# Kernel tuning notes

Measured on AMD Instinct MI355X. Metric: run time of the kernel, lower is better.

## Reference

```python
import jax, jax.numpy as jnp
import numpy as np

B, C, D, H, W = 8, 512, 512, 128, 128


def setup_inputs() -> dict:
    key = jax.random.key(0)
    ks = jax.random.split(key, 6)
    s = 0.02  # small init scale for stable softmax
    return {
        "x": jax.random.normal(ks[0], (B, C, H, W), dtype=jnp.float32),
        "context": jax.random.normal(ks[1], (B, D), dtype=jnp.float32),
        "Wq": jax.random.normal(ks[2], (C, D), dtype=jnp.float32) * s,
        "bq": jnp.ones((C,), dtype=jnp.float32),
        "Wk": jax.random.normal(ks[3], (C, C), dtype=jnp.float32) * s,
        "bk": jnp.zeros((C,), dtype=jnp.float32),
        "Wv": jax.random.normal(ks[4], (C, C), dtype=jnp.float32) * s,
        "bv": jnp.zeros((C,), dtype=jnp.float32),
    }


def reference(x, context, Wq, bq, Wk, bk, Wv, bv):
    # x: (B,C,H,W), context: (B,D)
    scale = x.shape[1] ** (-0.5)
    # q_proj: Linear(D -> C), single query per batch element
    q = context @ Wq.T + bq                      # (B, C)
    # 1x1 convs are channel-mixing GEMMs over the spatial grid
    k = jnp.einsum('bchw,oc->bohw', x, Wk) + bk[None, :, None, None]  # (B,C,H,W)
    v = jnp.einsum('bchw,oc->bohw', x, Wv) + bv[None, :, None, None]  # (B,C,H,W)
    # attention logits over the HW positions (query length == 1)
    logits = jnp.einsum('bc,bchw->bhw', q, k) * scale                 # (B,H,W)
    Bn, Hn, Wn = logits.shape
    attn = jax.nn.softmax(logits.reshape(Bn, Hn * Wn), axis=-1).reshape(Bn, Hn, Wn)
    # attention-pooled value -> channel gate
    gate = jnp.einsum('bhw,bchw->bc', attn, v)                        # (B,C)
    return x * gate[:, :, None, None]
```

## Files before the change

kernel.cpp:

```cpp
#include <hip/hip_runtime.h>
#include <math.h>

#define BB   8
#define CC   512
#define DD   512
#define HW   16384
#define HW4  4096


__global__ __launch_bounds__(256) void k_qproj(const float* __restrict__ ctx,
                                               const float* __restrict__ Wq,
                                               const float* __restrict__ bq,
                                               float* __restrict__ q) {
    int t = blockIdx.x * 256 + threadIdx.x;
    int b = t >> 9, c = t & (CC - 1);
    const float4* cr = (const float4*)(ctx + (size_t)b * DD);
    const float4* wr = (const float4*)(Wq + (size_t)c * DD);
    float acc = 0.f;
    #pragma unroll 8
    for (int d = 0; d < DD / 4; ++d) {
        float4 a = cr[d], w = wr[d];
        acc += a.x * w.x + a.y * w.y + a.z * w.z + a.w * w.w;
    }
    q[t] = acc + bq[c];
}

__global__ __launch_bounds__(256) void k_qk(const float* __restrict__ q,
                                            const float* __restrict__ Wk,
                                            float* __restrict__ qk) {
    __shared__ float qs[CC];
    int b = blockIdx.x >> 1;
    int c = (blockIdx.x & 1) * 256 + threadIdx.x;
    for (int i = threadIdx.x; i < CC; i += 256) qs[i] = q[b * CC + i];
    __syncthreads();
    float acc = 0.f;
    #pragma unroll 8
    for (int o = 0; o < CC; ++o) acc += qs[o] * Wk[(size_t)o * CC + c];
    qk[b * CC + c] = acc;
}

__global__ __launch_bounds__(256) void k_logits(const float* __restrict__ x,
                                                const float* __restrict__ qk,
                                                float* __restrict__ logits) {
    __shared__ float qs[CC];
    __shared__ float4 part[3][64];
    int b       = blockIdx.x >> 6;
    int hwchunk = blockIdx.x & 63;
    int wave = threadIdx.x >> 6, lane = threadIdx.x & 63;
    int hw4 = hwchunk * 64 + lane;
    for (int i = threadIdx.x; i < CC; i += 256) qs[i] = qk[b * CC + i];
    __syncthreads();
    const float4* x4 = (const float4*)x;
    size_t base = (size_t)b * CC * HW4 + (size_t)(wave * 128) * HW4 + hw4;
    float ax = 0.f, ay = 0.f, az = 0.f, aw = 0.f;
    #pragma unroll 8
    for (int c = 0; c < 128; ++c) {
        float4 v = x4[base + (size_t)c * HW4];
        float w = qs[wave * 128 + c];
        ax += w * v.x; ay += w * v.y; az += w * v.z; aw += w * v.w;
    }
    if (wave > 0) {
        float4 p = { ax, ay, az, aw };
        part[wave - 1][lane] = p;
    }
    __syncthreads();
    if (wave == 0) {
        #pragma unroll
        for (int w2 = 0; w2 < 3; ++w2) {
            float4 p = part[w2][lane];
            ax += p.x; ay += p.y; az += p.z; aw += p.w;
        }
        const float scale = 0.04419417382415922f;
        float4 o = { ax * scale, ay * scale, az * scale, aw * scale };
        ((float4*)logits)[(size_t)b * HW4 + hw4] = o;
    }
}

__global__ __launch_bounds__(1024) void k_softmax(float* __restrict__ buf) {
    int b = blockIdx.x, tid = threadIdx.x;
    float4* p4 = (float4*)(buf + (size_t)b * HW);
    float4 v[4];
    float m = -1e30f;
    #pragma unroll
    for (int i = 0; i < 4; ++i) {
        v[i] = p4[tid + i * 1024];
        m = fmaxf(m, fmaxf(fmaxf(v[i].x, v[i].y), fmaxf(v[i].z, v[i].w)));
    }
    __shared__ float redm[16], reds[16];
    for (int off = 32; off; off >>= 1) m = fmaxf(m, __shfl_down(m, off));
    if ((tid & 63) == 0) redm[tid >> 6] = m;
    __syncthreads();
    if (tid < 64) {
        float mm = (tid < 16) ? redm[tid] : -1e30f;
        for (int off = 8; off; off >>= 1) mm = fmaxf(mm, __shfl_down(mm, off));
        if (tid == 0) redm[0] = mm;
    }
    __syncthreads();
    m = redm[0];
    float s = 0.f;
    #pragma unroll
    for (int i = 0; i < 4; ++i) {
        v[i].x = expf(v[i].x - m); v[i].y = expf(v[i].y - m);
        v[i].z = expf(v[i].z - m); v[i].w = expf(v[i].w - m);
        s += v[i].x + v[i].y + v[i].z + v[i].w;
    }
    for (int off = 32; off; off >>= 1) s += __shfl_down(s, off);
    if ((tid & 63) == 0) reds[tid >> 6] = s;
    __syncthreads();
    if (tid < 64) {
        float ss = (tid < 16) ? reds[tid] : 0.f;
        for (int off = 8; off; off >>= 1) ss += __shfl_down(ss, off);
        if (tid == 0) reds[0] = ss;
    }
    __syncthreads();
    float inv = 1.f / reds[0];
    #pragma unroll
    for (int i = 0; i < 4; ++i) {
        float4 o = { v[i].x * inv, v[i].y * inv, v[i].z * inv, v[i].w * inv };
        p4[tid + i * 1024] = o;
    }
}

__global__ __launch_bounds__(256) void k_pool(const float* __restrict__ x,
                                              const float* __restrict__ attn,
                                              float* __restrict__ pooled) {
    int bc = blockIdx.x;
    int b  = bc >> 9;
    int tid = threadIdx.x;
    const float4* xr = (const float4*)x    + (size_t)bc * HW4;
    const float4* ar = (const float4*)attn + (size_t)b  * HW4;
    float acc = 0.f;
    #pragma unroll 8
    for (int i = tid; i < HW4; i += 256) {
        float4 xv = xr[i], av = ar[i];
        acc += xv.x * av.x + xv.y * av.y + xv.z * av.z + xv.w * av.w;
    }
    for (int off = 32; off; off >>= 1) acc += __shfl_down(acc, off);
    __shared__ float red[4];
    if ((tid & 63) == 0) red[tid >> 6] = acc;
    __syncthreads();
    if (tid == 0) pooled[bc] = red[0] + red[1] + red[2] + red[3];
}

__global__ __launch_bounds__(256) void k_gate(const float* __restrict__ pooled,
                                              const float* __restrict__ Wv,
                                              const float* __restrict__ bv,
                                              float* __restrict__ gate) {
    int t = blockIdx.x * 256 + threadIdx.x;
    int b = t >> 9, o = t & (CC - 1);
    const float4* pr = (const float4*)(pooled + (size_t)b * CC);
    const float4* wr = (const float4*)(Wv + (size_t)o * CC);
    float acc = 0.f;
    #pragma unroll 8
    for (int i = 0; i < CC / 4; ++i) {
        float4 p = pr[i], w = wr[i];
        acc += p.x * w.x + p.y * w.y + p.z * w.z + p.w * w.w;
    }
    gate[t] = acc + bv[o];
}

__global__ __launch_bounds__(256) void k_out(const float* __restrict__ x,
                                             const float* __restrict__ gate,
                                             float* __restrict__ out) {
    int bc = blockIdx.x;
    float g = gate[bc];
    const float4* xr = (const float4*)x   + (size_t)bc * HW4;
    float4*       orow = (float4*)out     + (size_t)bc * HW4;
    #pragma unroll 8
    for (int i = threadIdx.x; i < HW4; i += 256) {
        float4 v = xr[i];
        float4 o = { v.x * g, v.y * g, v.z * g, v.w * g };
        orow[i] = o;
    }
}

extern "C" void kernel_launch(void* const* d_in, const int* in_sizes, int n_in,
                              void* d_out, int out_size, void* d_ws, size_t ws_size,
                              hipStream_t stream) {
    const float* x   = (const float*)d_in[0];
    const float* ctx = (const float*)d_in[1];
    const float* Wq  = (const float*)d_in[2];
    const float* bq  = (const float*)d_in[3];
    const float* Wk  = (const float*)d_in[4];
    const float* Wv  = (const float*)d_in[6];
    const float* bv  = (const float*)d_in[7];
    float* out = (float*)d_out;

    float* ws     = (float*)d_ws;
    float* q      = ws;
    float* qk     = ws + 4096;
    float* pooled = ws + 8192;
    float* gate   = ws + 12288;
    float* logits = ws + 16384;

    k_qproj  <<<  16, 256, 0, stream>>>(ctx, Wq, bq, q);
    k_qk     <<<  16, 256, 0, stream>>>(q, Wk, qk);
    k_logits <<< 512, 256, 0, stream>>>(x, qk, logits);
    k_softmax<<<  BB,1024, 0, stream>>>(logits);
    k_pool   <<<4096, 256, 0, stream>>>(x, logits, pooled);
    k_gate   <<<  16, 256, 0, stream>>>(pooled, Wv, bv, gate);
    k_out    <<<4096, 256, 0, stream>>>(x, gate, out);
}
```

Before: 616.6 us.

## Fuse logits, softmax and pooling with per-chunk online-softmax partials

Replaces the logits, softmax and pooling kernels with one kernel. Each block computes its chunk of logits, a local max and exp-sum, and then re-reads its x tile (likely still in cache) to produce per-channel partial pooled sums. A small combine kernel rescales the chunk partials flash-attention style. This removes the separate full pass over x in k_pool and the logits round trip, at the cost of per-channel wave shuffle reductions and a 64-way partial buffer.

After: 643.2 us. 1.04x slower.

```diff
diff --git a/kernel.cpp b/kernel.cpp
--- a/kernel.cpp
+++ b/kernel.cpp
@@ -6,6 +6,7 @@
 #define DD   512
 #define HW   16384
 #define HW4  4096
+#define NCHUNK 64
 
 
 __global__ __launch_bounds__(256) void k_qproj(const float* __restrict__ ctx,
@@ -39,15 +40,18 @@
     qk[b * CC + c] = acc;
 }
 
-__global__ __launch_bounds__(256) void k_logits(const float* __restrict__ x,
-                                                const float* __restrict__ qk,
-                                                float* __restrict__ logits) {
-    __shared__ float qs[CC];
-    __shared__ float4 part[3][64];
-    int b       = blockIdx.x >> 6;
-    int hwchunk = blockIdx.x & 63;
+__global__ __launch_bounds__(256) void k_fused(const float* __restrict__ x,
+                                               const float* __restrict__ qk,
+                                               float* __restrict__ part,
+                                               float* __restrict__ stats) {
+    __shared__ float  qs[CC];
+    __shared__ float4 comb[3][64];
+    __shared__ float4 p4s[64];
+    __shared__ float  partLDS[CC];
+    int b     = blockIdx.x >> 6;
+    int chunk = blockIdx.x & 63;
     int wave = threadIdx.x >> 6, lane = threadIdx.x & 63;
-    int hw4 = hwchunk * 64 + lane;
+    int hw4 = chunk * 64 + lane;
     for (int i = threadIdx.x; i < CC; i += 256) qs[i] = qk[b * CC + i];
     __syncthreads();
     const float4* x4 = (const float4*)x;
@@ -61,85 +65,69 @@
     }
     if (wave > 0) {
         float4 p = { ax, ay, az, aw };
-        part[wave - 1][lane] = p;
+        comb[wave - 1][lane] = p;
     }
     __syncthreads();
     if (wave == 0) {
         #pragma unroll
         for (int w2 = 0; w2 < 3; ++w2) {
-            float4 p = part[w2][lane];
+            float4 p = comb[w2][lane];
             ax += p.x; ay += p.y; az += p.z; aw += p.w;
         }
         const float scale = 0.04419417382415922f;
-        float4 o = { ax * scale, ay * scale, az * scale, aw * scale };
-        ((float4*)logits)[(size_t)b * HW4 + hw4] = o;
+        ax *= scale; ay *= scale; az *= scale; aw *= scale;
+        float m = fmaxf(fmaxf(ax, ay), fmaxf(az, aw));
+        #pragma unroll
+        for (int off = 32; off; off >>= 1) m = fmaxf(m, __shfl_xor(m, off));
+        float4 p;
+        p.x = expf(ax - m); p.y = expf(ay - m);
+        p.z = expf(az - m); p.w = expf(aw - m);
+        float s = p.x + p.y + p.z + p.w;
+        #pragma unroll
+        for (int off = 32; off; off >>= 1) s += __shfl_xor(s, off);
+        p4s[lane] = p;
+        if (lane == 0) { stats[blockIdx.x * 2] = m; stats[blockIdx.x * 2 + 1] = s; }
     }
+    __syncthreads();
+    float4 pv = p4s[lane];
+    #pragma unroll 4
+    for (int c = 127; c >= 0; --c) {
+        float4 v = x4[base + (size_t)c * HW4];
+        float r = pv.x * v.x + pv.y * v.y + pv.z * v.z + pv.w * v.w;
+        #pragma unroll
+        for (int off = 32; off; off >>= 1) r += __shfl_down(r, off);
+        if (lane == 0) partLDS[wave * 128 + c] = r;
+    }
+    __syncthreads();
+    float4* pr = (float4*)(part + (size_t)blockIdx.x * CC);
+    for (int i = threadIdx.x; i < CC / 4; i += 256) pr[i] = ((float4*)partLDS)[i];
 }
 
-__global__ __launch_bounds__(1024) void k_softmax(float* __restrict__ buf) {
+__global__ __launch_bounds__(256) void k_combine(const float* __restrict__ part,
+                                                 const float* __restrict__ stats,
+                                                 float* __restrict__ pooled) {
+    __shared__ float wgt[NCHUNK];
     int b = blockIdx.x, tid = threadIdx.x;
-    float4* p4 = (float4*)(buf + (size_t)b * HW);
-    float4 v[4];
-    float m = -1e30f;
-    #pragma unroll
-    for (int i = 0; i < 4; ++i) {
-        v[i] = p4[tid + i * 1024];
-        m = fmaxf(m, fmaxf(fmaxf(v[i].x, v[i].y), fmaxf(v[i].z, v[i].w)));
-    }
-    __shared__ float redm[16], reds[16];
-    for (int off = 32; off; off >>= 1) m = fmaxf(m, __shfl_down(m, off));
-    if ((tid & 63) == 0) redm[tid >> 6] = m;
-    __syncthreads();
     if (tid < 64) {
-        float mm = (tid < 16) ? redm[tid] : -1e30f;
-        for (int off = 8; off; off >>= 1) mm = fmaxf(mm, __shfl_down(mm, off));
-        if (tid == 0) redm[0] = mm;
+        float mc = stats[(b * NCHUNK + tid) * 2];
+        float sc = stats[(b * NCHUNK + tid) * 2 + 1];
+        float m = mc;
+        #pragma unroll
+        for (int off = 32; off; off >>= 1) m = fmaxf(m, __shfl_xor(m, off));
+        float w = expf(mc - m);
+        float d = w * sc;
+        #pragma unroll
+        for (int off = 32; off; off >>= 1) d += __shfl_xor(d, off);
+        wgt[tid] = w / d;
     }
     __syncthreads();
-    m = redm[0];
-    float s = 0.f;
-    #pragma unroll
-    for (int i = 0; i < 4; ++i) {
-        v[i].x = expf(v[i].x - m); v[i].y = expf(v[i].y - m);
-        v[i].z = expf(v[i].z - m); v[i].w = expf(v[i].w - m);
-        s += v[i].x + v[i].y + v[i].z + v[i].w;
+    for (int c = tid; c < CC; c += 256) {
+        float acc = 0.f;
+        #pragma unroll 8
+        for (int ch = 0; ch < NCHUNK; ++ch)
+            acc += wgt[ch] * part[(size_t)(b * NCHUNK + ch) * CC + c];
+        pooled[b * CC + c] = acc;
     }
-    for (int off = 32; off; off >>= 1) s += __shfl_down(s, off);
-    if ((tid & 63) == 0) reds[tid >> 6] = s;
-    __syncthreads();
-    if (tid < 64) {
-        float ss = (tid < 16) ? reds[tid] : 0.f;
-        for (int off = 8; off; off >>= 1) ss += __shfl_down(ss, off);
-        if (tid == 0) reds[0] = ss;
-    }
-    __syncthreads();
-    float inv = 1.f / reds[0];
-    #pragma unroll
-    for (int i = 0; i < 4; ++i) {
-        float4 o = { v[i].x * inv, v[i].y * inv, v[i].z * inv, v[i].w * inv };
-        p4[tid + i * 1024] = o;
-    }
-}
-
-__global__ __launch_bounds__(256) void k_pool(const float* __restrict__ x,
-                                              const float* __restrict__ attn,
-                                              float* __restrict__ pooled) {
-    int bc = blockIdx.x;
-    int b  = bc >> 9;
-    int tid = threadIdx.x;
-    const float4* xr = (const float4*)x    + (size_t)bc * HW4;
-    const float4* ar = (const float4*)attn + (size_t)b  * HW4;
-    float acc = 0.f;
-    #pragma unroll 8
-    for (int i = tid; i < HW4; i += 256) {
-        float4 xv = xr[i], av = ar[i];
-        acc += xv.x * av.x + xv.y * av.y + xv.z * av.z + xv.w * av.w;
-    }
-    for (int off = 32; off; off >>= 1) acc += __shfl_down(acc, off);
-    __shared__ float red[4];
-    if ((tid & 63) == 0) red[tid >> 6] = acc;
-    __syncthreads();
-    if (tid == 0) pooled[bc] = red[0] + red[1] + red[2] + red[3];
 }
 
 __global__ __launch_bounds__(256) void k_gate(const float* __restrict__ pooled,
@@ -191,13 +179,13 @@
     float* qk     = ws + 4096;
     float* pooled = ws + 8192;
     float* gate   = ws + 12288;
-    float* logits = ws + 16384;
+    float* stats  = ws + 16384;
+    float* part   = ws + 17408;
 
     k_qproj  <<<  16, 256, 0, stream>>>(ctx, Wq, bq, q);
     k_qk     <<<  16, 256, 0, stream>>>(q, Wk, qk);
-    k_logits <<< 512, 256, 0, stream>>>(x, qk, logits);
-    k_softmax<<<  BB,1024, 0, stream>>>(logits);
-    k_pool   <<<4096, 256, 0, stream>>>(x, logits, pooled);
+    k_fused  <<< 512, 256, 0, stream>>>(x, qk, part, stats);
+    k_combine<<<  BB, 256, 0, stream>>>(part, stats, pooled);
     k_gate   <<<  16, 256, 0, stream>>>(pooled, Wv, bv, gate);
     k_out    <<<4096, 256, 0, stream>>>(x, gate, out);
 }
```
